# Performance work log

Measured on AMD Instinct MI355X. Metric: run time of the kernel, lower is better.

The kernel has to match this reference:

```python
import jax, jax.numpy as jnp
import numpy as np

NTOK, NINP, NREL = 50257, 512, 200
N, L, EPS = 1024, 64, 32  # n sequences, seq length, edges per sequence
E = N * EPS               # m.sum()


def setup_inputs() -> dict:
    key = jax.random.key(0)
    k1, k2, k3, k4 = jax.random.split(key, 4)
    seq = jax.random.randint(k1, (N, L), 0, NTOK, dtype=jnp.int32)
    m = jnp.full((N,), EPS, dtype=jnp.int32)          # edges per sequence (constant -> static E)
    rel = jax.random.randint(k2, (E,), 0, NREL, dtype=jnp.int32)
    emb = jax.random.normal(k3, (NTOK, NINP), dtype=jnp.float32)          # nn.Embedding weight
    W = 0.01 * jax.random.normal(k4, (NREL, NINP), dtype=jnp.float32)     # nn.Linear weight
    b = jnp.zeros((NREL,), dtype=jnp.float32)                             # nn.Linear bias
    return {"seq": seq, "m": m, "rel": rel, "emb": emb, "W": W, "b": b}


def reference(seq, m, rel, emb, W, b):
    # logit = linear(embedding(seq).sum(1))
    h = emb[seq].sum(axis=1)                    # (N, NINP) gather + segment-sum over tokens
    logit = h @ W.T + b                         # (N, NREL)

    # multi-label mask: mask[i, r] = True iff some edge of sequence i has relation r
    n_seq = m.shape[0]
    idx = jnp.repeat(jnp.arange(n_seq), m, total_repeat_length=rel.shape[0])  # (E,)
    mask = jnp.zeros((n_seq, logit.shape[1]), dtype=bool).at[idx, rel].set(True)

    # sum of logsigmoid on positive labels + log(1+1e-5 - sigmoid) on negatives, / len(seq)
    logp = jnp.sum(jnp.where(mask,
                             jax.nn.log_sigmoid(logit),
                             jnp.log(1.0 + 1e-5 - jax.nn.sigmoid(logit)))) / seq.shape[0]
    acc = jnp.mean(((logit > 0.5) == mask).astype(jnp.float32))
    return logp, acc
```

## Files before the change

kernel.cpp:

```cpp
#include <hip/hip_runtime.h>

#define NINP 512
#define NREL 200
#define LSEQ 64
#define WT_LD 256
#define SPB 2

__global__ __launch_bounds__(256) void wt_kernel(
    const float* __restrict__ W,
    float* __restrict__ Wt)
{
    const int b = blockIdx.x;
    const int t = threadIdx.x;
    #pragma unroll
    for (int j = 0; j < 2; ++j) {
        const int k = b * 2 + j;
        Wt[k * WT_LD + t] = (t < NREL) ? W[t * NINP + k] : 0.f;
    }
}

__global__ __launch_bounds__(1024) void fused_kernel(
    const int* __restrict__ seq,
    const float* __restrict__ emb,
    const float* __restrict__ Wt,
    const int* __restrict__ rel,
    const float* __restrict__ bias,
    float* __restrict__ out,
    int N, int eps)
{
    __shared__ int    toks[SPB * LSEQ];
    __shared__ float4 hpart[8][128];
    __shared__ float  h_lds[SPB][NINP];
    __shared__ unsigned int maskbits[SPB][8];
    __shared__ float  pd[SPB][4][256];
    __shared__ float  red_logp[16];
    __shared__ float  red_acc[16];

    const int i0 = blockIdx.x * SPB;
    const int t  = threadIdx.x;

    if (t < SPB * LSEQ) toks[t] = seq[i0 * LSEQ + t];
    if (t >= 512 && t < 512 + SPB * 8) ((unsigned int*)maskbits)[t - 512] = 0u;
    __syncthreads();

    const int g = t >> 7;
    const int e = t & 127;
    float4 acc = make_float4(0.f, 0.f, 0.f, 0.f);
    #pragma unroll
    for (int batch = 0; batch < 2; ++batch) {
        const int base = g * 16 + batch * 8;
        float4 v[8];
        #pragma unroll
        for (int j = 0; j < 8; ++j) {
            const int tok = __builtin_amdgcn_readfirstlane(toks[base + j]);
            v[j] = ((const float4*)(emb + (long)tok * NINP))[e];
        }
        float4 s01, s23, s45, s67;
        s01.x = v[0].x + v[1].x; s01.y = v[0].y + v[1].y; s01.z = v[0].z + v[1].z; s01.w = v[0].w + v[1].w;
        s23.x = v[2].x + v[3].x; s23.y = v[2].y + v[3].y; s23.z = v[2].z + v[3].z; s23.w = v[2].w + v[3].w;
        s45.x = v[4].x + v[5].x; s45.y = v[4].y + v[5].y; s45.z = v[4].z + v[5].z; s45.w = v[4].w + v[5].w;
        s67.x = v[6].x + v[7].x; s67.y = v[6].y + v[7].y; s67.z = v[6].z + v[7].z; s67.w = v[6].w + v[7].w;
        acc.x += (s01.x + s23.x) + (s45.x + s67.x);
        acc.y += (s01.y + s23.y) + (s45.y + s67.y);
        acc.z += (s01.z + s23.z) + (s45.z + s67.z);
        acc.w += (s01.w + s23.w) + (s45.w + s67.w);
    }
    hpart[g][e] = acc;
    __syncthreads();

    if (t < SPB * 128) {
        const int s = t >> 7, ee = t & 127;
        float4 a0 = hpart[4 * s + 0][ee];
        float4 a1 = hpart[4 * s + 1][ee];
        float4 a2 = hpart[4 * s + 2][ee];
        float4 a3 = hpart[4 * s + 3][ee];
        float4 c;
        c.x = (a0.x + a1.x) + (a2.x + a3.x);
        c.y = (a0.y + a1.y) + (a2.y + a3.y);
        c.z = (a0.z + a1.z) + (a2.z + a3.z);
        c.w = (a0.w + a1.w) + (a2.w + a3.w);
        ((float4*)h_lds)[t] = c;
    }
    if (t >= 512 && t < 512 + SPB * 32) {
        const int s = (t - 512) >> 5, j = (t - 512) & 31;
        if (j < eps) {
            int r = rel[(i0 + s) * eps + j];
            atomicOr(&maskbits[s][r >> 5], 1u << (r & 31));
        }
    }
    __syncthreads();

    const int kslice = t >> 8;
    const int r      = t & 255;
    float d0 = 0.f, d1 = 0.f;
    const float4* h40 = (const float4*)h_lds[0];
    const float4* h41 = (const float4*)h_lds[1];
    #pragma unroll 4
    for (int k4 = kslice * 32; k4 < kslice * 32 + 32; ++k4) {
        const int k = k4 * 4;
        const float w0 = Wt[(k + 0) * WT_LD + r];
        const float w1 = Wt[(k + 1) * WT_LD + r];
        const float w2 = Wt[(k + 2) * WT_LD + r];
        const float w3 = Wt[(k + 3) * WT_LD + r];
        const float4 hv0 = h40[k4];
        const float4 hv1 = h41[k4];
        d0 += w0 * hv0.x + w1 * hv0.y + w2 * hv0.z + w3 * hv0.w;
        d1 += w0 * hv1.x + w1 * hv1.y + w2 * hv1.z + w3 * hv1.w;
    }
    pd[0][kslice][r] = d0;
    pd[1][kslice][r] = d1;
    __syncthreads();

    float term = 0.f, match = 0.f;
    if (t < NREL) {
        const float bt = bias[t];
        #pragma unroll
        for (int s = 0; s < SPB; ++s) {
            const float dot = ((pd[s][0][t] + pd[s][1][t]) +
                               (pd[s][2][t] + pd[s][3][t])) + bt;
            const unsigned mb = (maskbits[s][t >> 5] >> (t & 31)) & 1u;
            float tr;
            if (mb) {
                tr = fminf(dot, 0.f) - log1pf(expf(-fabsf(dot)));
            } else {
                tr = logf(1e-5f + 1.f / (1.f + expf(dot)));
            }
            term  += tr;
            match += (((dot > 0.5f) ? 1u : 0u) == mb) ? 1.f : 0.f;
        }
    }

    #pragma unroll
    for (int off = 32; off > 0; off >>= 1) {
        term  += __shfl_down(term,  off);
        match += __shfl_down(match, off);
    }
    const int wave = t >> 6;
    const int lane = t & 63;
    if (lane == 0) { red_logp[wave] = term; red_acc[wave] = match; }
    __syncthreads();
    if (t == 0) {
        float s = 0.f, a = 0.f;
        #pragma unroll
        for (int w = 0; w < 16; ++w) { s += red_logp[w]; a += red_acc[w]; }
        atomicAdd(out + 0, s / (float)N);
        atomicAdd(out + 1, a / ((float)N * (float)NREL));
    }
}

extern "C" void kernel_launch(void* const* d_in, const int* in_sizes, int n_in,
                              void* d_out, int out_size, void* d_ws, size_t ws_size,
                              hipStream_t stream) {
    const int*   seq = (const int*)d_in[0];
    const int*   m   = (const int*)d_in[1]; (void)m;
    const int*   rel = (const int*)d_in[2];
    const float* emb = (const float*)d_in[3];
    const float* W   = (const float*)d_in[4];
    const float* b   = (const float*)d_in[5];
    float* out = (float*)d_out;

    const int N   = in_sizes[1];
    const int eps = in_sizes[2] / N;

    float* Wt = (float*)d_ws;

    hipMemsetAsync(out, 0, 2 * sizeof(float), stream);
    wt_kernel<<<NINP / 2, 256, 0, stream>>>(W, Wt);
    fused_kernel<<<N / SPB, 1024, 0, stream>>>(seq, emb, Wt, rel, b, out, N, eps);
}
```

Baseline: 181.9 us.

## Process four sequences per block and register-tile the GEMV over sequences

Doubles sequences per block to 4, so each Wt float4 load is reused across four sequences through a packed h layout in LDS. Each wave gathers 16 full embedding rows as two float4 halves. The dot product now splits K across 16 waves, each lane computing 4 relations by 4 sequences, followed by a 16-way LDS reduction. This halves the grid to 256 blocks and cuts per-block Wt traffic per sequence, at the cost of more LDS use, a reduction step and fewer blocks to fill the GPU.

```diff
diff --git a/kernel.cpp b/kernel.cpp
--- a/kernel.cpp
+++ b/kernel.cpp
@@ -4,7 +4,7 @@
 #define NREL 200
 #define LSEQ 64
 #define WT_LD 256
-#define SPB 2
+#define SPB 4
 
 __global__ __launch_bounds__(256) void wt_kernel(
     const float* __restrict__ W,
@@ -29,104 +29,118 @@
     int N, int eps)
 {
     __shared__ int    toks[SPB * LSEQ];
-    __shared__ float4 hpart[8][128];
-    __shared__ float  h_lds[SPB][NINP];
+    __shared__ float4 hpart[16][2][64];
+    __shared__ float  h_pack[NINP][SPB];
+    __shared__ float4 pd[16][SPB][64];
     __shared__ unsigned int maskbits[SPB][8];
-    __shared__ float  pd[SPB][4][256];
-    __shared__ float  red_logp[16];
-    __shared__ float  red_acc[16];
+    __shared__ float  red_lp[16], red_ac[16];
 
-    const int i0 = blockIdx.x * SPB;
-    const int t  = threadIdx.x;
+    const int i0   = blockIdx.x * SPB;
+    const int t    = threadIdx.x;
+    const int wave = t >> 6;
+    const int lane = t & 63;
 
     if (t < SPB * LSEQ) toks[t] = seq[i0 * LSEQ + t];
-    if (t >= 512 && t < 512 + SPB * 8) ((unsigned int*)maskbits)[t - 512] = 0u;
+    if (t < SPB * 8) ((unsigned int*)maskbits)[t] = 0u;
     __syncthreads();
 
-    const int g = t >> 7;
-    const int e = t & 127;
-    float4 acc = make_float4(0.f, 0.f, 0.f, 0.f);
-    #pragma unroll
-    for (int batch = 0; batch < 2; ++batch) {
-        const int base = g * 16 + batch * 8;
-        float4 v[8];
-        #pragma unroll
-        for (int j = 0; j < 8; ++j) {
-            const int tok = __builtin_amdgcn_readfirstlane(toks[base + j]);
-            v[j] = ((const float4*)(emb + (long)tok * NINP))[e];
-        }
-        float4 s01, s23, s45, s67;
-        s01.x = v[0].x + v[1].x; s01.y = v[0].y + v[1].y; s01.z = v[0].z + v[1].z; s01.w = v[0].w + v[1].w;
-        s23.x = v[2].x + v[3].x; s23.y = v[2].y + v[3].y; s23.z = v[2].z + v[3].z; s23.w = v[2].w + v[3].w;
-        s45.x = v[4].x + v[5].x; s45.y = v[4].y + v[5].y; s45.z = v[4].z + v[5].z; s45.w = v[4].w + v[5].w;
-        s67.x = v[6].x + v[7].x; s67.y = v[6].y + v[7].y; s67.z = v[6].z + v[7].z; s67.w = v[6].w + v[7].w;
-        acc.x += (s01.x + s23.x) + (s45.x + s67.x);
-        acc.y += (s01.y + s23.y) + (s45.y + s67.y);
-        acc.z += (s01.z + s23.z) + (s45.z + s67.z);
-        acc.w += (s01.w + s23.w) + (s45.w + s67.w);
-    }
-    hpart[g][e] = acc;
-    __syncthreads();
-
-    if (t < SPB * 128) {
-        const int s = t >> 7, ee = t & 127;
-        float4 a0 = hpart[4 * s + 0][ee];
-        float4 a1 = hpart[4 * s + 1][ee];
-        float4 a2 = hpart[4 * s + 2][ee];
-        float4 a3 = hpart[4 * s + 3][ee];
-        float4 c;
-        c.x = (a0.x + a1.x) + (a2.x + a3.x);
-        c.y = (a0.y + a1.y) + (a2.y + a3.y);
-        c.z = (a0.z + a1.z) + (a2.z + a3.z);
-        c.w = (a0.w + a1.w) + (a2.w + a3.w);
-        ((float4*)h_lds)[t] = c;
-    }
-    if (t >= 512 && t < 512 + SPB * 32) {
-        const int s = (t - 512) >> 5, j = (t - 512) & 31;
+    if (t < SPB * 32) {
+        const int s = t >> 5, j = t & 31;
         if (j < eps) {
             int r = rel[(i0 + s) * eps + j];
             atomicOr(&maskbits[s][r >> 5], 1u << (r & 31));
         }
     }
+
+    {
+        const int rbase = (wave >> 2) * LSEQ + (wave & 3) * 16;
+        float4 lo = make_float4(0.f, 0.f, 0.f, 0.f);
+        float4 hi = lo;
+        #pragma unroll
+        for (int j0 = 0; j0 < 16; j0 += 4) {
+            const float* r0 = emb + (long)__builtin_amdgcn_readfirstlane(toks[rbase + j0 + 0]) * NINP;
+            const float* r1 = emb + (long)__builtin_amdgcn_readfirstlane(toks[rbase + j0 + 1]) * NINP;
+            const float* r2 = emb + (long)__builtin_amdgcn_readfirstlane(toks[rbase + j0 + 2]) * NINP;
+            const float* r3 = emb + (long)__builtin_amdgcn_readfirstlane(toks[rbase + j0 + 3]) * NINP;
+            float4 l0 = ((const float4*)r0)[lane];
+            float4 h0 = ((const float4*)r0)[64 + lane];
+            float4 l1 = ((const float4*)r1)[lane];
+            float4 h1 = ((const float4*)r1)[64 + lane];
+            float4 l2 = ((const float4*)r2)[lane];
+            float4 h2 = ((const float4*)r2)[64 + lane];
+            float4 l3 = ((const float4*)r3)[lane];
+            float4 h3 = ((const float4*)r3)[64 + lane];
+            lo.x += (l0.x + l1.x) + (l2.x + l3.x);
+            lo.y += (l0.y + l1.y) + (l2.y + l3.y);
+            lo.z += (l0.z + l1.z) + (l2.z + l3.z);
+            lo.w += (l0.w + l1.w) + (l2.w + l3.w);
+            hi.x += (h0.x + h1.x) + (h2.x + h3.x);
+            hi.y += (h0.y + h1.y) + (h2.y + h3.y);
+            hi.z += (h0.z + h1.z) + (h2.z + h3.z);
+            hi.w += (h0.w + h1.w) + (h2.w + h3.w);
+        }
+        hpart[wave][0][lane] = lo;
+        hpart[wave][1][lane] = hi;
+    }
     __syncthreads();
 
-    const int kslice = t >> 8;
-    const int r      = t & 255;
-    float d0 = 0.f, d1 = 0.f;
-    const float4* h40 = (const float4*)h_lds[0];
-    const float4* h41 = (const float4*)h_lds[1];
-    #pragma unroll 4
-    for (int k4 = kslice * 32; k4 < kslice * 32 + 32; ++k4) {
-        const int k = k4 * 4;
-        const float w0 = Wt[(k + 0) * WT_LD + r];
-        const float w1 = Wt[(k + 1) * WT_LD + r];
-        const float w2 = Wt[(k + 2) * WT_LD + r];
-        const float w3 = Wt[(k + 3) * WT_LD + r];
-        const float4 hv0 = h40[k4];
-        const float4 hv1 = h41[k4];
-        d0 += w0 * hv0.x + w1 * hv0.y + w2 * hv0.z + w3 * hv0.w;
-        d1 += w0 * hv1.x + w1 * hv1.y + w2 * hv1.z + w3 * hv1.w;
+    {
+        float2 v;
+        #pragma unroll
+        for (int d = 0; d < 2; ++d) {
+            const int idx = 2 * t + d;
+            const int s = idx & 3;
+            const int k = idx >> 2;
+            const int f = k >> 2, c = k & 3;
+            const int half = f >> 6, lf = f & 63;
+            float sum = 0.f;
+            #pragma unroll
+            for (int q = 0; q < 4; ++q)
+                sum += ((const float*)&hpart[s * 4 + q][half][lf])[c];
+            ((float*)&v)[d] = sum;
+        }
+        ((float2*)h_pack)[t] = v;
     }
-    pd[0][kslice][r] = d0;
-    pd[1][kslice][r] = d1;
+    __syncthreads();
+
+    {
+        const float4* Wt4 = (const float4*)Wt;
+        float4 a0 = make_float4(0.f, 0.f, 0.f, 0.f);
+        float4 a1 = a0, a2 = a0, a3 = a0;
+        const int kbase = wave * 32;
+        #pragma unroll 4
+        for (int k = kbase; k < kbase + 32; ++k) {
+            const float4 wv = Wt4[k * 64 + lane];
+            const float4 hp = ((const float4*)h_pack)[k];
+            a0.x += hp.x * wv.x; a0.y += hp.x * wv.y; a0.z += hp.x * wv.z; a0.w += hp.x * wv.w;
+            a1.x += hp.y * wv.x; a1.y += hp.y * wv.y; a1.z += hp.y * wv.z; a1.w += hp.y * wv.w;
+            a2.x += hp.z * wv.x; a2.y += hp.z * wv.y; a2.z += hp.z * wv.z; a2.w += hp.z * wv.w;
+            a3.x += hp.w * wv.x; a3.y += hp.w * wv.y; a3.z += hp.w * wv.z; a3.w += hp.w * wv.w;
+        }
+        pd[wave][0][lane] = a0;
+        pd[wave][1][lane] = a1;
+        pd[wave][2][lane] = a2;
+        pd[wave][3][lane] = a3;
+    }
     __syncthreads();
 
     float term = 0.f, match = 0.f;
-    if (t < NREL) {
-        const float bt = bias[t];
-        #pragma unroll
-        for (int s = 0; s < SPB; ++s) {
-            const float dot = ((pd[s][0][t] + pd[s][1][t]) +
-                               (pd[s][2][t] + pd[s][3][t])) + bt;
-            const unsigned mb = (maskbits[s][t >> 5] >> (t & 31)) & 1u;
-            float tr;
+    {
+        const int s = t >> 8;
+        const int r = t & 255;
+        if (r < NREL) {
+            const int f = r >> 2, c = r & 3;
+            float dot = bias[r];
+            #pragma unroll
+            for (int w = 0; w < 16; ++w)
+                dot += ((const float*)&pd[w][s][f])[c];
+            const unsigned mb = (maskbits[s][r >> 5] >> (r & 31)) & 1u;
             if (mb) {
-                tr = fminf(dot, 0.f) - log1pf(expf(-fabsf(dot)));
+                term = fminf(dot, 0.f) - log1pf(expf(-fabsf(dot)));
             } else {
-                tr = logf(1e-5f + 1.f / (1.f + expf(dot)));
+                term = logf(1e-5f + 1.f / (1.f + expf(dot)));
             }
-            term  += tr;
-            match += (((dot > 0.5f) ? 1u : 0u) == mb) ? 1.f : 0.f;
+            match = (((dot > 0.5f) ? 1u : 0u) == mb) ? 1.f : 0.f;
         }
     }
 
@@ -135,14 +149,12 @@
         term  += __shfl_down(term,  off);
         match += __shfl_down(match, off);
     }
-    const int wave = t >> 6;
-    const int lane = t & 63;
-    if (lane == 0) { red_logp[wave] = term; red_acc[wave] = match; }
+    if (lane == 0) { red_lp[wave] = term; red_ac[wave] = match; }
     __syncthreads();
     if (t == 0) {
         float s = 0.f, a = 0.f;
         #pragma unroll
-        for (int w = 0; w < 16; ++w) { s += red_logp[w]; a += red_acc[w]; }
+        for (int w = 0; w < 16; ++w) { s += red_lp[w]; a += red_ac[w]; }
         atomicAdd(out + 0, s / (float)N);
         atomicAdd(out + 1, a / ((float)N * (float)NREL));
     }
```

New measurement: 169.6 us. 6.8% less time.
